# Performance work log

Measured on AMD Instinct MI355X. Metric: run time of the kernel, lower is better.

## Reference

```python
import jax, jax.numpy as jnp
import numpy as np

N_POINTS = 16384  # matches init_kwargs n_points


def setup_inputs() -> dict:
    key = jax.random.key(0)
    k1, k2 = jax.random.split(key)
    B, N = 32, 524288
    p = jax.random.normal(k1, (B, N, 3), dtype=jnp.float32)
    zero_mask = jax.random.bernoulli(k2, 0.3, (B, N))
    p = jnp.where(zero_mask[..., None], 0.0, p)
    return {"pred_cloud": p}


def _sample_one(key, p):
    # p: (N, 3). Torch: non_zeros = sum(p, dim=2).ne(0); filter, then
    # randperm[:n] if enough points else randint with replacement.
    N = p.shape[0]
    mask = jnp.sum(p, axis=1) != 0              # (N,) valid points
    k = jnp.sum(mask).astype(jnp.int32)          # number of valid points
    # stable argsort puts valid (False for ~mask) indices first -> compacted index list
    order = jnp.argsort(~mask, stable=True)      # (N,)
    kperm, krep = jax.random.split(key)
    # branch A (k >= n_points): random subset without replacement among valid
    scores = jnp.where(mask, jax.random.uniform(kperm, (N,)), jnp.inf)
    perm_idx = jnp.argsort(scores)[:N_POINTS]    # (n_points,) valid indices, random order
    # branch B (k < n_points): randint(0, k) with replacement over compacted valid ids
    u = jax.random.uniform(krep, (N_POINTS,))
    rep = jnp.floor(u * k.astype(u.dtype)).astype(jnp.int32) % jnp.maximum(k, 1)
    repl_idx = order[rep]
    idx = jnp.where(k < N_POINTS, repl_idx, perm_idx)  # (n_points,)
    return p[idx]                                 # (n_points, 3)


def reference(pred_cloud):
    B = pred_cloud.shape[0]
    keys = jax.random.split(jax.random.key(42), B)
    return jax.vmap(_sample_one)(keys, pred_cloud)  # (B, n_points, 3)
```

## Files before the change

### kernel.cpp

```cpp
#include <hip/hip_runtime.h>
#include <stdint.h>

#define NB 32
#define NN 524288
#define NPTS 16384
#define NBLK (NN / 1024)
#define BCAP 96
#define SCAP 20480
#define NBINS 4096
#define THRESH 0.0478515625f

struct Keys { uint32_t k[2 * NB]; };

__host__ __device__ static inline void tf2x32(uint32_t k0, uint32_t k1,
                                              uint32_t x0, uint32_t x1,
                                              uint32_t* o0, uint32_t* o1) {
  uint32_t ks2 = k0 ^ k1 ^ 0x1BD11BDAu;
  x0 += k0; x1 += k1;
#define TFR(r) { x0 += x1; x1 = (x1 << (r)) | (x1 >> (32 - (r))); x1 ^= x0; }
  TFR(13) TFR(15) TFR(26) TFR(6)
  x0 += k1; x1 += ks2 + 1u;
  TFR(17) TFR(29) TFR(16) TFR(24)
  x0 += ks2; x1 += k0 + 2u;
  TFR(13) TFR(15) TFR(26) TFR(6)
  x0 += k0; x1 += k1 + 3u;
  TFR(17) TFR(29) TFR(16) TFR(24)
  x0 += k1; x1 += ks2 + 4u;
  TFR(13) TFR(15) TFR(26) TFR(6)
  x0 += ks2; x1 += k0 + 5u;
#undef TFR
  *o0 = x0; *o1 = x1;
}

__global__ __launch_bounds__(256) void k_candidates(
    const float* __restrict__ p, Keys keys,
    uint64_t* __restrict__ cand, uint32_t* __restrict__ blkcnt) {
  const int b = blockIdx.y;
  const int bx = blockIdx.x;
  const int t = threadIdx.x;
  const int i0 = (bx * 256 + t) * 4;
  const uint32_t kp0 = keys.k[2 * b], kp1 = keys.k[2 * b + 1];
  const float* pb = p + (size_t)b * NN * 3;
  typedef float f2 __attribute__((ext_vector_type(2), aligned(4)));

  uint64_t mykeys[4];
  int nc = 0;
#pragma unroll
  for (int j = 0; j < 4; ++j) {
    uint32_t o0, o1;
    tf2x32(kp0, kp1, 0u, (uint32_t)(i0 + j), &o0, &o1);
    uint32_t bits = o0 ^ o1;
    float u = __uint_as_float((bits >> 9) | 0x3F800000u) - 1.0f;
    if (u < THRESH) {
      const float* pp = pb + 3 * (size_t)(i0 + j);
      f2 v = *(const f2*)pp;
      float z = pp[2];
      if (((v.x + v.y) + z) != 0.0f)
        mykeys[nc++] = ((uint64_t)__float_as_uint(u) << 32) | (uint32_t)(i0 + j);
    }
  }

  __shared__ uint32_t lcnt;
  if (t == 0) lcnt = 0u;
  __syncthreads();
  uint32_t loc = 0u;
  if (nc) loc = atomicAdd(&lcnt, (uint32_t)nc);
  __syncthreads();
  uint64_t* cb = cand + ((size_t)b * NBLK + bx) * BCAP;
  for (int j = 0; j < nc; ++j) {
    uint32_t sl = loc + j;
    if (sl < BCAP) cb[sl] = mykeys[j];
  }
  if (t == 0) blkcnt[b * NBLK + bx] = (lcnt > BCAP) ? BCAP : lcnt;
}

__global__ __launch_bounds__(1024) void k_scan_scatter(
    const uint64_t* __restrict__ cand, const uint32_t* __restrict__ blkcnt,
    uint32_t* __restrict__ cum, uint32_t* __restrict__ scount,
    uint64_t* __restrict__ sorted) {
  const int b = blockIdx.x;
  const int t = threadIdx.x;
  const int lane = t & 63, wave = t >> 6;
  __shared__ uint32_t lhist[NBINS];
  __shared__ uint32_t lcum[NBINS + 1];
  __shared__ uint32_t wsum[16];
  __shared__ uint32_t lc[NBLK];

  for (int i = t; i < NBINS; i += 1024) lhist[i] = 0u;
  if (t < NBLK) {
    uint32_t M = blkcnt[b * NBLK + t];
    lc[t] = (M > BCAP) ? BCAP : M;
  }
  __syncthreads();

  {
    const int r = t >> 1;
    const uint32_t M = lc[r];
    const uint64_t* cb = cand + ((size_t)b * NBLK + r) * BCAP;
    for (uint32_t j = (uint32_t)(t & 1); j < M; j += 2) {
      uint32_t ub = (uint32_t)(cb[j] >> 32);
      atomicAdd(&lhist[(int)(__uint_as_float(ub) * 65536.0f)], 1u);
    }
  }
  __syncthreads();

  uint32_t h0 = lhist[4 * t], h1 = lhist[4 * t + 1],
           h2 = lhist[4 * t + 2], h3 = lhist[4 * t + 3];
  uint32_t s4 = h0 + h1 + h2 + h3;
  uint32_t v = s4;
  for (int off = 1; off < 64; off <<= 1) {
    uint32_t n = __shfl_up(v, off, 64);
    if (lane >= off) v += n;
  }
  if (lane == 63) wsum[wave] = v;
  __syncthreads();
  if (t < 16) {
    uint32_t w = wsum[t];
    for (int off = 1; off < 16; off <<= 1) {
      uint32_t n = __shfl_up(w, off, 64);
      if (t >= off) w += n;
    }
    wsum[t] = w;
  }
  __syncthreads();
  uint32_t incl = v + (wave ? wsum[wave - 1] : 0u);
  uint32_t c[5];
  c[0] = incl - s4; c[1] = c[0] + h0; c[2] = c[1] + h1;
  c[3] = c[2] + h2; c[4] = incl;
  lcum[4 * t] = c[0]; lcum[4 * t + 1] = c[1];
  lcum[4 * t + 2] = c[2]; lcum[4 * t + 3] = c[3];
  if (t == 1023) lcum[NBINS] = incl;
  uint32_t* gc = cum + (size_t)b * (NBINS + 1);
  gc[4 * t] = c[0]; gc[4 * t + 1] = c[1];
  gc[4 * t + 2] = c[2]; gc[4 * t + 3] = c[3];
  if (t == 1023) gc[NBINS] = incl;
#pragma unroll
  for (int q = 0; q < 4; ++q)
    if (c[q] < NPTS && c[q + 1] >= NPTS) {
      uint32_t sc = c[q + 1];
      scount[b] = (sc > SCAP) ? SCAP : sc;
    }
  if (t == 1023 && incl < NPTS) scount[b] = incl;

  for (int i = t; i < NBINS; i += 1024) lhist[i] = 0u;
  __syncthreads();
  {
    const int r = t >> 1;
    const uint32_t M = lc[r];
    const uint64_t* cb = cand + ((size_t)b * NBLK + r) * BCAP;
    for (uint32_t j = (uint32_t)(t & 1); j < M; j += 2) {
      uint64_t key = cb[j];
      int bin = (int)(__uint_as_float((uint32_t)(key >> 32)) * 65536.0f);
      uint32_t c0 = lcum[bin];
      if (c0 < NPTS) {
        uint32_t pos = atomicAdd(&lhist[bin], 1u);
        uint32_t sl = c0 + pos;
        if (sl < SCAP) sorted[(size_t)b * SCAP + sl] = key;
      }
    }
  }
}

__global__ __launch_bounds__(256) void k_rank(
    const float* __restrict__ p, const uint64_t* __restrict__ sorted,
    const uint32_t* __restrict__ cum, const uint32_t* __restrict__ scount,
    float* __restrict__ out) {
  const int b = blockIdx.y;
  const uint32_t j = blockIdx.x * 256 + threadIdx.x;
  if (j >= scount[b]) return;
  const uint64_t* sb = sorted + (size_t)b * SCAP;
  uint64_t key = sb[j];
  float u = __uint_as_float((uint32_t)(key >> 32));
  int bin = (int)(u * 65536.0f);
  const uint32_t* gc = cum + (size_t)b * (NBINS + 1);
  uint32_t c0 = gc[bin], c1 = gc[bin + 1];
  uint32_t r = c0;
  for (uint32_t l = c0; l < c1; ++l) r += (sb[l] < key) ? 1u : 0u;
  if (r < NPTS) {
    uint32_t idx = (uint32_t)key;
    const float* pp = p + (size_t)b * NN * 3 + 3 * (size_t)idx;
    float* o = out + ((size_t)b * NPTS + r) * 3;
    o[0] = pp[0]; o[1] = pp[1]; o[2] = pp[2];
  }
}

extern "C" void kernel_launch(void* const* d_in, const int* in_sizes, int n_in,
                              void* d_out, int out_size, void* d_ws, size_t ws_size,
                              hipStream_t stream) {
  const float* p = (const float*)d_in[0];
  float* out = (float*)d_out;
  uint8_t* ws = (uint8_t*)d_ws;

  size_t off_cand   = 0;
  size_t off_sorted = off_cand + (size_t)NB * NBLK * BCAP * 8;
  size_t off_cum    = off_sorted + (size_t)NB * SCAP * 8;
  size_t off_scnt   = off_cum + (size_t)NB * (NBINS + 1) * 4;
  size_t off_bcnt   = off_scnt + 128;

  uint64_t* cand   = (uint64_t*)(ws + off_cand);
  uint64_t* sorted = (uint64_t*)(ws + off_sorted);
  uint32_t* cum    = (uint32_t*)(ws + off_cum);
  uint32_t* scount = (uint32_t*)(ws + off_scnt);
  uint32_t* blkcnt = (uint32_t*)(ws + off_bcnt);

  Keys keys;
  for (int b = 0; b < NB; ++b) {
    uint32_t kb0, kb1, kp0, kp1;
    tf2x32(0u, 42u, 0u, (uint32_t)b, &kb0, &kb1);
    tf2x32(kb0, kb1, 0u, 0u, &kp0, &kp1);
    keys.k[2 * b] = kp0; keys.k[2 * b + 1] = kp1;
  }

  dim3 g1(NBLK, NB);
  k_candidates<<<g1, 256, 0, stream>>>(p, keys, cand, blkcnt);
  k_scan_scatter<<<NB, 1024, 0, stream>>>(cand, blkcnt, cum, scount, sorted);
  dim3 g4(SCAP / 256, NB);
  k_rank<<<g4, 256, 0, stream>>>(p, sorted, cum, scount, out);
}
```

Baseline: 311.6 us.

## Fuse scan-scatter and rank kernels into one per-batch finish kernel

Merges the rank-and-gather stage into the scan/scatter kernel, so each batch's 1024-thread block ranks its own sorted candidates using the cumulative histogram held in shared memory. This drops one kernel launch and the global writes and reads of the cumulative array and the selected count. In exchange, the rank stage now runs on only 32 blocks instead of a grid of 80×32 blocks, which reduces parallelism for the gather and rank loop.

New measurement: 354.7 us. 1.14x slower.

```diff
diff --git a/kernel.cpp b/kernel.cpp
--- a/kernel.cpp
+++ b/kernel.cpp
@@ -74,10 +74,10 @@
   if (t == 0) blkcnt[b * NBLK + bx] = (lcnt > BCAP) ? BCAP : lcnt;
 }
 
-__global__ __launch_bounds__(1024) void k_scan_scatter(
-    const uint64_t* __restrict__ cand, const uint32_t* __restrict__ blkcnt,
-    uint32_t* __restrict__ cum, uint32_t* __restrict__ scount,
-    uint64_t* __restrict__ sorted) {
+__global__ __launch_bounds__(1024) void k_finish(
+    const float* __restrict__ p, const uint64_t* __restrict__ cand,
+    const uint32_t* __restrict__ blkcnt, uint64_t* __restrict__ sorted,
+    float* __restrict__ out) {
   const int b = blockIdx.x;
   const int t = threadIdx.x;
   const int lane = t & 63, wave = t >> 6;
@@ -85,6 +85,7 @@
   __shared__ uint32_t lcum[NBINS + 1];
   __shared__ uint32_t wsum[16];
   __shared__ uint32_t lc[NBLK];
+  __shared__ uint32_t ssc;
 
   for (int i = t; i < NBINS; i += 1024) lhist[i] = 0u;
   if (t < NBLK) {
@@ -130,20 +131,17 @@
   lcum[4 * t] = c[0]; lcum[4 * t + 1] = c[1];
   lcum[4 * t + 2] = c[2]; lcum[4 * t + 3] = c[3];
   if (t == 1023) lcum[NBINS] = incl;
-  uint32_t* gc = cum + (size_t)b * (NBINS + 1);
-  gc[4 * t] = c[0]; gc[4 * t + 1] = c[1];
-  gc[4 * t + 2] = c[2]; gc[4 * t + 3] = c[3];
-  if (t == 1023) gc[NBINS] = incl;
 #pragma unroll
   for (int q = 0; q < 4; ++q)
     if (c[q] < NPTS && c[q + 1] >= NPTS) {
       uint32_t sc = c[q + 1];
-      scount[b] = (sc > SCAP) ? SCAP : sc;
-    }
-  if (t == 1023 && incl < NPTS) scount[b] = incl;
+      ssc = (sc > SCAP) ? SCAP : sc;
+    }
+  if (t == 1023 && incl < NPTS) ssc = incl;
 
   for (int i = t; i < NBINS; i += 1024) lhist[i] = 0u;
   __syncthreads();
+  uint64_t* sb = sorted + (size_t)b * SCAP;
   {
     const int r = t >> 1;
     const uint32_t M = lc[r];
@@ -155,32 +153,26 @@
       if (c0 < NPTS) {
         uint32_t pos = atomicAdd(&lhist[bin], 1u);
         uint32_t sl = c0 + pos;
-        if (sl < SCAP) sorted[(size_t)b * SCAP + sl] = key;
+        if (sl < SCAP) sb[sl] = key;
       }
     }
   }
-}
-
-__global__ __launch_bounds__(256) void k_rank(
-    const float* __restrict__ p, const uint64_t* __restrict__ sorted,
-    const uint32_t* __restrict__ cum, const uint32_t* __restrict__ scount,
-    float* __restrict__ out) {
-  const int b = blockIdx.y;
-  const uint32_t j = blockIdx.x * 256 + threadIdx.x;
-  if (j >= scount[b]) return;
-  const uint64_t* sb = sorted + (size_t)b * SCAP;
-  uint64_t key = sb[j];
-  float u = __uint_as_float((uint32_t)(key >> 32));
-  int bin = (int)(u * 65536.0f);
-  const uint32_t* gc = cum + (size_t)b * (NBINS + 1);
-  uint32_t c0 = gc[bin], c1 = gc[bin + 1];
-  uint32_t r = c0;
-  for (uint32_t l = c0; l < c1; ++l) r += (sb[l] < key) ? 1u : 0u;
-  if (r < NPTS) {
-    uint32_t idx = (uint32_t)key;
-    const float* pp = p + (size_t)b * NN * 3 + 3 * (size_t)idx;
-    float* o = out + ((size_t)b * NPTS + r) * 3;
-    o[0] = pp[0]; o[1] = pp[1]; o[2] = pp[2];
+  __syncthreads();
+
+  const uint32_t nsc = ssc;
+  const float* pbb = p + (size_t)b * NN * 3;
+  float* ob = out + (size_t)b * NPTS * 3;
+  for (uint32_t j = t; j < nsc; j += 1024) {
+    uint64_t key = sb[j];
+    int bin = (int)(__uint_as_float((uint32_t)(key >> 32)) * 65536.0f);
+    uint32_t c0 = lcum[bin], c1 = lcum[bin + 1];
+    uint32_t r = c0;
+    for (uint32_t l = c0; l < c1; ++l) r += (sb[l] < key) ? 1u : 0u;
+    if (r < NPTS) {
+      const float* pp = pbb + 3 * (size_t)(uint32_t)key;
+      float* o = ob + 3 * (size_t)r;
+      o[0] = pp[0]; o[1] = pp[1]; o[2] = pp[2];
+    }
   }
 }
 
@@ -193,14 +185,10 @@
 
   size_t off_cand   = 0;
   size_t off_sorted = off_cand + (size_t)NB * NBLK * BCAP * 8;
-  size_t off_cum    = off_sorted + (size_t)NB * SCAP * 8;
-  size_t off_scnt   = off_cum + (size_t)NB * (NBINS + 1) * 4;
-  size_t off_bcnt   = off_scnt + 128;
+  size_t off_bcnt   = off_sorted + (size_t)NB * SCAP * 8;
 
   uint64_t* cand   = (uint64_t*)(ws + off_cand);
   uint64_t* sorted = (uint64_t*)(ws + off_sorted);
-  uint32_t* cum    = (uint32_t*)(ws + off_cum);
-  uint32_t* scount = (uint32_t*)(ws + off_scnt);
   uint32_t* blkcnt = (uint32_t*)(ws + off_bcnt);
 
   Keys keys;
@@ -213,7 +201,5 @@
 
   dim3 g1(NBLK, NB);
   k_candidates<<<g1, 256, 0, stream>>>(p, keys, cand, blkcnt);
-  k_scan_scatter<<<NB, 1024, 0, stream>>>(cand, blkcnt, cum, scount, sorted);
-  dim3 g4(SCAP / 256, NB);
-  k_rank<<<g4, 256, 0, stream>>>(p, sorted, cum, scount, out);
-}
+  k_finish<<<NB, 1024, 0, stream>>>(p, cand, blkcnt, sorted, out);
+}
```
